# Optimization experiments

Measured on AMD Instinct MI355X. Metric: run time of the kernel, lower is better.

The kernel has to match this reference:

```python
import jax, jax.numpy as jnp
import numpy as np

# Window-batch of 16x16 windows from a U-Net stage
B, C, H, W = 128, 128, 16, 16
HEADS = 8
EQK, EV = 128, 512      # embed_dim_qk, embed_dim_v (embed_dim=512, ratio=4)
L = H * W               # tokens per window (stride=1)


def _conv3x3(x, w, b):
    # NCHW 3x3 conv, padding 1
    out = jax.lax.conv_general_dilated(x, w, (1, 1), ((1, 1), (1, 1)),
                                       dimension_numbers=('NCHW', 'OIHW', 'NCHW'))
    return out + b[None, :, None, None]


def _pos_att(q, wq, bq, wk, bk, wv, bv, wo, bo, gamma):
    # MultiHeadAttention2D_POS, stride=1 -> conv_q/k/v are 1x1 convs
    hd, hdv = EQK // HEADS, EV // HEADS

    def proj(x, w, bias, d):
        y = jnp.einsum('bchw,ec->behw', x, w) + bias[None, :, None, None]
        return y.reshape(B, HEADS, d, L).transpose(0, 1, 3, 2)  # (B,h,L,d)

    pq = proj(q, wq, bq, hd)
    pk = proj(q, wk, bk, hd)
    pv = proj(q, wv, bv, hdv)
    attn = jax.nn.softmax(jnp.einsum('bhqd,bhkd->bhqk', pq, pk) * hd ** -0.5, axis=-1)
    out = jnp.einsum('bhqk,bhkd->bhqd', attn, pv)
    out = out.transpose(0, 1, 3, 2).reshape(B, EV, H, W)
    out = _conv3x3(out, wo, bo)             # proj_out: 3x3 conv EV->C
    return q + out * gamma                  # gamma-scaled residual


def _cha_att(q, wq, bq, wk, bk, wv, bv, wo, bo, gamma):
    # MultiHeadAttention2D_CHA: depthwise 1x1 grouped convs (channel multiplier = HEADS),
    # attention over the CHANNEL axis. Faithfully reproduces torch's reshape of the
    # group-major (c*HEADS+h) channel layout into (B, heads, C, L).
    def dwproj(x, w, bias):
        y = (x[:, :, None] * w.reshape(C, HEADS)[None, :, :, None, None]
             + bias.reshape(C, HEADS)[None, :, :, None, None])
        return y.reshape(B, C * HEADS, H, W).reshape(B, HEADS, C, L)

    pq = dwproj(q, wq, bq)
    pk = dwproj(q, wk, bk)
    pv = dwproj(q, wv, bv)
    attn = jax.nn.softmax(jnp.einsum('bhcl,bhdl->bhcd', pq, pk) * L ** -0.5, axis=-1)
    out = jnp.einsum('bhcd,bhdl->bhcl', attn, pv)      # (B,h,C,L)
    out = out.reshape(B, HEADS * C, H, W)
    # proj_out: grouped 1x1 ConvTranspose (== grouped 1x1 conv): sum each HEADS-sized group
    out = (out.reshape(B, C, HEADS, H, W)
           * wo.reshape(C, HEADS)[None, :, :, None, None]).sum(2) + bo[None, :, None, None]
    return q + out * gamma


def _forward(qkv_pos, qkv_cha,
             pos_wq, pos_bq, pos_wk, pos_bk, pos_wv, pos_bv, pos_wo, pos_bo, gamma_pos,
             cha_wq, cha_bq, cha_wk, cha_bk, cha_wv, cha_bv, cha_wo, cha_bo, gamma_cha,
             fuse_w, fuse_b):
    out_pos = _pos_att(qkv_pos, pos_wq, pos_bq, pos_wk, pos_bk, pos_wv, pos_bv,
                       pos_wo, pos_bo, gamma_pos)
    out_cha = _cha_att(qkv_cha, cha_wq, cha_bq, cha_wk, cha_bk, cha_wv, cha_bv,
                       cha_wo, cha_bo, gamma_cha)
    out = (out_pos + out_cha) * 0.5          # att_fusion='add' (slides=0 -> full slices)
    return _conv3x3(out, fuse_w, fuse_b)     # conv_out (Dropout2d is identity at eval)


def setup_inputs() -> dict:
    key = jax.random.key(0)
    ks = jax.random.split(key, 24)
    n = lambda k, shape, s=0.05: jax.random.normal(k, shape, dtype=jnp.float32) * s
    return {
        'qkv_pos': jax.random.normal(ks[0], (B, C, H, W), jnp.float32),
        'qkv_cha': jax.random.normal(ks[1], (B, C, H, W), jnp.float32),
        'pos_wq': n(ks[2], (EQK, C)), 'pos_bq': n(ks[3], (EQK,)),
        'pos_wk': n(ks[4], (EQK, C)), 'pos_bk': n(ks[5], (EQK,)),
        'pos_wv': n(ks[6], (EV, C)), 'pos_bv': n(ks[7], (EV,)),
        'pos_wo': n(ks[8], (C, EV, 3, 3)), 'pos_bo': n(ks[9], (C,)),
        'gamma_pos': jnp.array(0.1, jnp.float32),
        'cha_wq': n(ks[10], (C * HEADS,)), 'cha_bq': n(ks[11], (C * HEADS,)),
        'cha_wk': n(ks[12], (C * HEADS,)), 'cha_bk': n(ks[13], (C * HEADS,)),
        'cha_wv': n(ks[14], (C * HEADS,)), 'cha_bv': n(ks[15], (C * HEADS,)),
        'cha_wo': n(ks[16], (C * HEADS,)), 'cha_bo': n(ks[17], (C,)),
        'gamma_cha': jnp.array(0.1, jnp.float32),
        'fuse_w': n(ks[18], (C, C, 3, 3)), 'fuse_b': n(ks[19], (C,)),
    }


def reference(qkv_pos, qkv_cha,
              pos_wq, pos_bq, pos_wk, pos_bk, pos_wv, pos_bv, pos_wo, pos_bo, gamma_pos,
              cha_wq, cha_bq, cha_wk, cha_bk, cha_wv, cha_bv, cha_wo, cha_bo, gamma_cha,
              fuse_w, fuse_b):
    return _forward(qkv_pos, qkv_cha,
                    pos_wq, pos_bq, pos_wk, pos_bk, pos_wv, pos_bv, pos_wo, pos_bo, gamma_pos,
                    cha_wq, cha_bq, cha_wk, cha_bk, cha_wv, cha_bv, cha_wo, cha_bo, gamma_cha,
                    fuse_w, fuse_b)
```

## Files before the change

### kernel.cpp

```cpp
#include <hip/hip_runtime.h>
#include <cstdint>
#include <cstddef>

typedef unsigned short ushort_t;
typedef unsigned int uint_t;
typedef __attribute__((ext_vector_type(8))) short bf16x8;
typedef __attribute__((ext_vector_type(4))) float f32x4;

#define NB 128
#define NC 128
#define NL 256
#define NH 8
#define HD 16
#define HDV 64
#define NEV 512
#define PHALF 4194304

__device__ __forceinline__ ushort_t f2bf(float f) {
    uint_t u = __float_as_uint(f);
    u += 0x7fffu + ((u >> 16) & 1u);
    return (ushort_t)(u >> 16);
}
__device__ __forceinline__ float bf2f(ushort_t s) {
    return __uint_as_float(((uint_t)s) << 16);
}
__device__ __forceinline__ uint_t pack2(float lo, float hi) {
    uint_t r;
    asm("v_cvt_pk_bf16_f32 %0, %1, %2" : "=v"(r) : "v"(lo), "v"(hi));
    return r;
}

template<int CIN>
__global__ __launch_bounds__(256) void k_wpack(const float* __restrict__ w,
                                               short* __restrict__ wp) {
    int idx = blockIdx.x * 256 + threadIdx.x;
    if (idx >= CIN * 1152) return;
    int j    = idx & 7;
    int lane = (idx >> 3) & 63;
    int frag = idx >> 9;
    int rt   = frag & 7;
    int tap  = (frag >> 3) % 9;
    int ch   = frag / 72;
    int co   = rt * 16 + (lane & 15);
    int g    = lane >> 4;
    int ci   = ch * 32 + g * 8 + j;
    wp[idx] = (short)f2bf(w[((size_t)co * CIN + ci) * 9 + tap]);
}

template<int E>
__global__ __launch_bounds__(256) void k_wpack_qkv(const float* __restrict__ w,
                                                   short* __restrict__ wp) {
    int idx = blockIdx.x * 256 + threadIdx.x;
    if (idx >= E * 128) return;
    int j    = idx & 7;
    int lane = (idx >> 3) & 63;
    int ch   = (idx >> 9) & 3;
    int rt   = idx >> 11;
    int n = lane & 15, g = lane >> 4;
    wp[idx] = (short)f2bf(w[(size_t)(rt*16 + n)*128 + ch*32 + g*8 + j]);
}

__global__ __launch_bounds__(256) void k_xpose(const float* __restrict__ x,
                                               ushort_t* __restrict__ xbf) {
    const int half = blockIdx.x, b = blockIdx.y, t = threadIdx.x;
    const float* src = x + (size_t)b*NC*NL + (size_t)half*64*NL + t;
    uint_t* dst = (uint_t*)(xbf + ((size_t)b*NL + t)*NC + half*64);
    #pragma unroll
    for (int k8 = 0; k8 < 8; ++k8) {
        uint4 u;
        u.x = pack2(src[(k8*8+0)*NL], src[(k8*8+1)*NL]);
        u.y = pack2(src[(k8*8+2)*NL], src[(k8*8+3)*NL]);
        u.z = pack2(src[(k8*8+4)*NL], src[(k8*8+5)*NL]);
        u.w = pack2(src[(k8*8+6)*NL], src[(k8*8+7)*NL]);
        *(uint4*)(dst + k8*4) = u;
    }
}

__global__ __launch_bounds__(512, 4) void k_pos_mfma(
    const ushort_t* __restrict__ xbf,
    const short* __restrict__ wpq, const short* __restrict__ wpk,
    const short* __restrict__ wpv,
    const float* __restrict__ bq, const float* __restrict__ bk,
    const float* __restrict__ bv,
    ushort_t* __restrict__ att)
{
    const int h = blockIdx.x, b = blockIdx.y;
    const int t = threadIdx.x;
    const int lane = t & 63, w = t >> 6;
    const int n = lane & 15, g = lane >> 4;

    __shared__ __align__(16) short lds[26112];

    const f32x4 z4 = {0.f, 0.f, 0.f, 0.f};
    f32x4 qacc[2], kacc[2], vacc[4][2];
    #pragma unroll
    for (int ct = 0; ct < 2; ++ct) { qacc[ct] = z4; kacc[ct] = z4; }
    #pragma unroll
    for (int vt = 0; vt < 4; ++vt)
        #pragma unroll
        for (int ct = 0; ct < 2; ++ct) vacc[vt][ct] = z4;

    const ushort_t* xr = xbf + ((size_t)(b*NL + w*32 + n))*NC;

    #pragma unroll 2
    for (int ch = 0; ch < 4; ++ch) {
        bf16x8 xb[2];
        #pragma unroll
        for (int ct = 0; ct < 2; ++ct)
            xb[ct] = *(const bf16x8*)(xr + ct*16*NC + ch*32 + g*8);
        const size_t fo = ((size_t)((h*4 + ch)*64) + lane) * 8;
        {
            bf16x8 aq = *(const bf16x8*)(wpq + fo);
            #pragma unroll
            for (int ct = 0; ct < 2; ++ct)
                qacc[ct] = __builtin_amdgcn_mfma_f32_16x16x32_bf16(aq, xb[ct], qacc[ct], 0, 0, 0);
        }
        {
            bf16x8 ak = *(const bf16x8*)(wpk + fo);
            #pragma unroll
            for (int ct = 0; ct < 2; ++ct)
                kacc[ct] = __builtin_amdgcn_mfma_f32_16x16x32_bf16(ak, xb[ct], kacc[ct], 0, 0, 0);
        }
        #pragma unroll
        for (int vt = 0; vt < 4; ++vt) {
            bf16x8 av = *(const bf16x8*)(wpv + ((size_t)((((h*4 + vt)*4) + ch)*64) + lane) * 8);
            #pragma unroll
            for (int ct = 0; ct < 2; ++ct)
                vacc[vt][ct] = __builtin_amdgcn_mfma_f32_16x16x32_bf16(xb[ct], av, vacc[vt][ct], 0, 0, 0);
        }
    }

    uint_t qu01[2], qu23[2];
    {
        float bqv[4], bkv[4];
        #pragma unroll
        for (int r = 0; r < 4; ++r) {
            bqv[r] = bq[h*16 + g*4 + r];
            bkv[r] = bk[h*16 + g*4 + r];
        }
        #pragma unroll
        for (int ct = 0; ct < 2; ++ct) {
            qu01[ct] = pack2(qacc[ct][0] + bqv[0], qacc[ct][1] + bqv[1]);
            qu23[ct] = pack2(qacc[ct][2] + bqv[2], qacc[ct][3] + bqv[3]);
            uint2 kp;
            kp.x = pack2(kacc[ct][0] + bkv[0], kacc[ct][1] + bkv[1]);
            kp.y = pack2(kacc[ct][2] + bkv[2], kacc[ct][3] + bkv[3]);
            *(uint2*)&lds[(w*32 + ct*16 + n)*16 + g*4] = kp;
        }
        #pragma unroll
        for (int vt = 0; vt < 4; ++vt) {
            const float bvv = bv[h*64 + vt*16 + n];
            #pragma unroll
            for (int ct = 0; ct < 2; ++ct) {
                uint2 vp;
                vp.x = pack2(vacc[vt][ct][0] + bvv, vacc[vt][ct][1] + bvv);
                vp.y = pack2(vacc[vt][ct][2] + bvv, vacc[vt][ct][3] + bvv);
                *(uint2*)&lds[9216 + (vt*16 + n)*264 + w*32 + ct*16 + g*4] = vp;
            }
        }
    }
    __syncthreads();

    const int a0 = (n + 32*(g & 1)) * 4;
    #pragma unroll 1
    for (int qt = 0; qt < 2; ++qt) {
        union { uint_t u[4]; bf16x8 v; } qfu;
        qfu.u[0] = (uint_t)__builtin_amdgcn_ds_bpermute(a0,      (int)qu01[qt]);
        qfu.u[1] = (uint_t)__builtin_amdgcn_ds_bpermute(a0,      (int)qu23[qt]);
        qfu.u[2] = (uint_t)__builtin_amdgcn_ds_bpermute(a0 + 64, (int)qu01[qt]);
        qfu.u[3] = (uint_t)__builtin_amdgcn_ds_bpermute(a0 + 64, (int)qu23[qt]);
        if (g >= 2) { qfu.u[0] = 0; qfu.u[1] = 0; qfu.u[2] = 0; qfu.u[3] = 0; }
        bf16x8 qf = qfu.v;

        f32x4 s[16];
        #pragma unroll
        for (int kt = 0; kt < 16; ++kt) {
            bf16x8 kf = (bf16x8){0,0,0,0,0,0,0,0};
            if (g < 2) kf = *(const bf16x8*)&lds[(kt*16 + n)*16 + g*8];
            s[kt] = __builtin_amdgcn_mfma_f32_16x16x32_bf16(kf, qf, z4, 0, 0, 0);
        }
        float den = 0.f;
        #pragma unroll
        for (int kt = 0; kt < 16; ++kt)
            #pragma unroll
            for (int r = 0; r < 4; ++r) {
                float e = exp2f(s[kt][r] * 0.36067376022224085f);
                s[kt][r] = e;
                den += e;
            }
        den += __shfl_xor(den, 16);
        den += __shfl_xor(den, 32);
        const float inv = 1.f / den;

        f32x4 oacc[4] = {z4, z4, z4, z4};
        #pragma unroll
        for (int c2 = 0; c2 < 8; ++c2) {
            #pragma unroll
            for (int u = 0; u < 2; ++u) {
                const int kt = 2*c2 + u;
                uint2 pp;
                pp.x = pack2(s[kt][0], s[kt][1]);
                pp.y = pack2(s[kt][2], s[kt][3]);
                *(uint2*)&lds[4096 + w*640 + n*40 + u*16 + g*4] = pp;
            }
            bf16x8 pf = *(const bf16x8*)&lds[4096 + w*640 + n*40 + g*8];
            #pragma unroll
            for (int vt = 0; vt < 4; ++vt) {
                bf16x8 av = *(const bf16x8*)&lds[9216 + (vt*16 + n)*264 + c2*32 + g*8];
                oacc[vt] = __builtin_amdgcn_mfma_f32_16x16x32_bf16(av, pf, oacc[vt], 0, 0, 0);
            }
        }
        ushort_t* ap = att + (((size_t)b*NL + (w*32 + qt*16 + n))*NEV + h*HDV + g*4);
        #pragma unroll
        for (int vt = 0; vt < 4; ++vt) {
            uint2 op;
            op.x = pack2(oacc[vt][0]*inv, oacc[vt][1]*inv);
            op.y = pack2(oacc[vt][2]*inv, oacc[vt][3]*inv);
            *(uint2*)(ap + vt*16) = op;
        }
    }
}

__global__ __launch_bounds__(256, 3) void k_conv_ci(
    const ushort_t* __restrict__ att, const short* __restrict__ wp,
    ushort_t* __restrict__ P)
{
    const int kc = blockIdx.x >> 1, lh = blockIdx.x & 1, b = blockIdx.y;
    const int t = threadIdx.x;
    const int lane = t & 63, w = t >> 6;
    const int wr = w >> 1, wc = w & 1;
    const int n = lane & 15, gl = lane >> 4;
    const int y0 = lh * 8;

    __shared__ __align__(16) short ims[2][5760];

    {
        bf16x8 z = {0,0,0,0,0,0,0,0};
        bf16x8* p = (bf16x8*)&ims[0][0];
        for (int i = t; i < 1440; i += 256) p[i] = z;
    }

    f32x4 acc[4][4];
    #pragma unroll
    for (int i = 0; i < 4; ++i)
        #pragma unroll
        for (int j = 0; j < 4; ++j) acc[i][j] = (f32x4){0.f,0.f,0.f,0.f};

    const int gg1 = t & 3,        xx1 = (t >> 2) & 15,        yp1 = t >> 6;
    const int id2 = t + 256;
    const int gg2 = id2 & 3,      xx2 = (id2 >> 2) & 15,      yp2 = id2 >> 6;
    const int id3 = t + 512;
    const int gg3 = id3 & 3,      xx3 = (id3 >> 2) & 15,      yp3 = id3 >> 6;
    const bool has3 = (t < 128);
    const int y1 = y0 - 1 + yp1, y2 = y0 - 1 + yp2, y3 = y0 - 1 + yp3;
    const bool ok1 = (y1 >= 0) && (y1 < 16);
    const bool ok2 = (y2 >= 0) && (y2 < 16);
    const bool ok3 = has3 && (y3 >= 0) && (y3 < 16);
    const ushort_t* src1 = att + ((size_t)(b*NL + y1*16 + xx1))*NEV + kc*256 + gg1*8;
    const ushort_t* src2 = att + ((size_t)(b*NL + y2*16 + xx2))*NEV + kc*256 + gg2*8;
    const ushort_t* src3 = att + ((size_t)(b*NL + y3*16 + xx3))*NEV + kc*256 + gg3*8;
    const int slot1 = ((yp1*4 + gg1)*18 + xx1 + 1) * 8;
    const int slot2 = ((yp2*4 + gg2)*18 + xx2 + 1) * 8;
    const int slot3 = ((yp3*4 + gg3)*18 + xx3 + 1) * 8;

    bf16x8 v1 = {0,0,0,0,0,0,0,0}, v2 = v1, v3 = v1;
    if (ok1) v1 = *(const bf16x8*)src1;
    if (ok2) v2 = *(const bf16x8*)src2;
    if (ok3) v3 = *(const bf16x8*)src3;
    __syncthreads();

    #pragma unroll 1
    for (int ch = 0; ch < 8; ++ch) {
        short* buf = &ims[ch & 1][0];
        *(bf16x8*)&buf[slot1] = v1;
        *(bf16x8*)&buf[slot2] = v2;
        if (has3) *(bf16x8*)&buf[slot3] = v3;
        if (ch < 7) {
            if (ok1) v1 = *(const bf16x8*)(src1 + (ch + 1) * 32);
            if (ok2) v2 = *(const bf16x8*)(src2 + (ch + 1) * 32);
            if (ok3) v3 = *(const bf16x8*)(src3 + (ch + 1) * 32);
        }
        __syncthreads();
        #pragma unroll
        for (int tap = 0; tap < 9; ++tap) {
            const int dy = tap / 3, dx = tap % 3;
            bf16x8 Bf[4];
            #pragma unroll
            for (int ct = 0; ct < 4; ++ct)
                Bf[ct] = *(const bf16x8*)&buf[(((wc*4 + ct + dy)*4 + gl)*18 + n + dx) * 8];
            bf16x8 Af[4];
            #pragma unroll
            for (int rt = 0; rt < 4; ++rt)
                Af[rt] = *(const bf16x8*)(wp +
                    ((size_t)(((kc*8 + ch)*9 + tap)*8 + wr*4 + rt)) * 512 + lane*8);
            #pragma unroll
            for (int rt = 0; rt < 4; ++rt)
                #pragma unroll
                for (int ct = 0; ct < 4; ++ct)
                    acc[rt][ct] = __builtin_amdgcn_mfma_f32_16x16x32_bf16(
                        Af[rt], Bf[ct], acc[rt][ct], 0, 0, 0);
        }
    }

    ushort_t* Pb = P + (size_t)kc * PHALF + (size_t)b * NL * NC;
    #pragma unroll
    for (int rt = 0; rt < 4; ++rt) {
        const int co0 = wr*64 + rt*16 + gl*4;
        #pragma unroll
        for (int ct = 0; ct < 4; ++ct) {
            const int l = lh*128 + wc*64 + ct*16 + n;
            uint2 u;
            u.x = pack2(acc[rt][ct][0], acc[rt][ct][1]);
            u.y = pack2(acc[rt][ct][2], acc[rt][ct][3]);
            *(uint2*)(Pb + (size_t)l*NC + co0) = u;
        }
    }
}

__global__ __launch_bounds__(256, 3) void k_conv_co(
    const float* __restrict__ comb, const short* __restrict__ wp,
    const float* __restrict__ bias, float* __restrict__ out)
{
    const int kc = blockIdx.x >> 1, lh = blockIdx.x & 1, b = blockIdx.y;
    const int t = threadIdx.x;
    const int lane = t & 63, w = t >> 6;
    const int wr = w >> 1, wc = w & 1;
    const int n = lane & 15, gl = lane >> 4;
    const int y0 = lh * 8;

    __shared__ __align__(16) short ims[2][5760];

    {
        bf16x8 z = {0,0,0,0,0,0,0,0};
        bf16x8* p = (bf16x8*)&ims[0][0];
        for (int i = t; i < 1440; i += 256) p[i] = z;
    }

    f32x4 acc[2][4];
    #pragma unroll
    for (int i = 0; i < 2; ++i)
        #pragma unroll
        for (int j = 0; j < 4; ++j) acc[i][j] = (f32x4){0.f,0.f,0.f,0.f};

    const int gg1 = t & 3,        xx1 = (t >> 2) & 15,        yp1 = t >> 6;
    const int id2 = t + 256;
    const int gg2 = id2 & 3,      xx2 = (id2 >> 2) & 15,      yp2 = id2 >> 6;
    const int id3 = t + 512;
    const int gg3 = id3 & 3,      xx3 = (id3 >> 2) & 15,      yp3 = id3 >> 6;
    const bool has3 = (t < 128);
    const int y1 = y0 - 1 + yp1, y2 = y0 - 1 + yp2, y3 = y0 - 1 + yp3;
    const bool ok1 = (y1 >= 0) && (y1 < 16);
    const bool ok2 = (y2 >= 0) && (y2 < 16);
    const bool ok3 = has3 && (y3 >= 0) && (y3 < 16);
    const float* s1 = comb + ((size_t)(b*NL + y1*16 + xx1))*NC + gg1*8;
    const float* s2 = comb + ((size_t)(b*NL + y2*16 + xx2))*NC + gg2*8;
    const float* s3 = comb + ((size_t)(b*NL + y3*16 + xx3))*NC + gg3*8;
    const int slot1 = ((yp1*4 + gg1)*18 + xx1 + 1) * 8;
    const int slot2 = ((yp2*4 + gg2)*18 + xx2 + 1) * 8;
    const int slot3 = ((yp3*4 + gg3)*18 + xx3 + 1) * 8;

    float4 f1a, f1b, f2a, f2b, f3a, f3b;
    f1a = f1b = f2a = f2b = f3a = f3b = (float4){0.f,0.f,0.f,0.f};
    if (ok1) { f1a = *(const float4*)s1; f1b = *(const float4*)(s1 + 4); }
    if (ok2) { f2a = *(const float4*)s2; f2b = *(const float4*)(s2 + 4); }
    if (ok3) { f3a = *(const float4*)s3; f3b = *(const float4*)(s3 + 4); }
    __syncthreads();

    #pragma unroll 1
    for (int ch = 0; ch < 4; ++ch) {
        short* buf = &ims[ch & 1][0];
        uint4 w1, w2, w3;
        w1.x = pack2(f1a.x, f1a.y);  w1.y = pack2(f1a.z, f1a.w);
        w1.z = pack2(f1b.x, f1b.y);  w1.w = pack2(f1b.z, f1b.w);
        w2.x = pack2(f2a.x, f2a.y);  w2.y = pack2(f2a.z, f2a.w);
        w2.z = pack2(f2b.x, f2b.y);  w2.w = pack2(f2b.z, f2b.w);
        w3.x = pack2(f3a.x, f3a.y);  w3.y = pack2(f3a.z, f3a.w);
        w3.z = pack2(f3b.x, f3b.y);  w3.w = pack2(f3b.z, f3b.w);
        *(uint4*)&buf[slot1] = w1;
        *(uint4*)&buf[slot2] = w2;
        if (has3) *(uint4*)&buf[slot3] = w3;
        if (ch < 3) {
            if (ok1) { f1a = *(const float4*)(s1 + (ch+1)*32); f1b = *(const float4*)(s1 + (ch+1)*32 + 4); }
            if (ok2) { f2a = *(const float4*)(s2 + (ch+1)*32); f2b = *(const float4*)(s2 + (ch+1)*32 + 4); }
            if (ok3) { f3a = *(const float4*)(s3 + (ch+1)*32); f3b = *(const float4*)(s3 + (ch+1)*32 + 4); }
        }
        __syncthreads();
        #pragma unroll
        for (int tap = 0; tap < 9; ++tap) {
            const int dy = tap / 3, dx = tap % 3;
            bf16x8 Bf[4];
            #pragma unroll
            for (int ct = 0; ct < 4; ++ct)
                Bf[ct] = *(const bf16x8*)&buf[(((wc*4 + ct + dy)*4 + gl)*18 + n + dx) * 8];
            bf16x8 Af[2];
            #pragma unroll
            for (int rt = 0; rt < 2; ++rt)
                Af[rt] = *(const bf16x8*)(wp +
                    ((size_t)((ch*9 + tap)*8 + kc*4 + wr*2 + rt)) * 512 + lane*8);
            #pragma unroll
            for (int rt = 0; rt < 2; ++rt)
                #pragma unroll
                for (int ct = 0; ct < 4; ++ct)
                    acc[rt][ct] = __builtin_amdgcn_mfma_f32_16x16x32_bf16(
                        Af[rt], Bf[ct], acc[rt][ct], 0, 0, 0);
        }
    }

    #pragma unroll
    for (int rt = 0; rt < 2; ++rt) {
        const int co0 = kc*64 + wr*32 + rt*16 + gl*4;
        const float c0 = bias[co0+0], c1 = bias[co0+1],
                    c2 = bias[co0+2], c3 = bias[co0+3];
        #pragma unroll
        for (int ct = 0; ct < 4; ++ct) {
            const int l = lh*128 + wc*64 + ct*16 + n;
            f32x4 a = acc[rt][ct];
            out[((size_t)b*NC + co0+0)*NL + l] = c0 + a[0];
            out[((size_t)b*NC + co0+1)*NL + l] = c1 + a[1];
            out[((size_t)b*NC + co0+2)*NL + l] = c2 + a[2];
            out[((size_t)b*NC + co0+3)*NL + l] = c3 + a[3];
        }
    }
}

#define NLP 260
__global__ __launch_bounds__(256) void k_cha(
    const float* __restrict__ xc,
    const float* __restrict__ cwq, const float* __restrict__ cbq,
    const float* __restrict__ cwk, const float* __restrict__ cbk,
    const float* __restrict__ cwv, const float* __restrict__ cbv,
    const float* __restrict__ cwo, const float* __restrict__ cbo,
    const float* __restrict__ gamma,
    const ushort_t* __restrict__ P, const float* __restrict__ qpos,
    const float* __restrict__ pbo, const float* __restrict__ gpos,
    float* __restrict__ comb)
{
    const int h = blockIdx.x, b = blockIdx.y, t = threadIdx.x;
    __shared__ float qh[16][NLP];
    __shared__ float G_s[16][17];
    __shared__ float S_s[16];
    __shared__ float wq_s[128], bq_s[128], wk_s[128], bk_s[128], wv_s[128], bv_s[128];
    __shared__ float A_s[128][17];
    __shared__ float B_s[128];
    __shared__ float M_s[16][17];
    __shared__ float c_s[16];

    #pragma unroll
    for (int j = 0; j < 16; ++j)
        qh[j][t] = xc[((size_t)b*NC + h*16 + j)*NL + t];
    if (t < 128) {
        const int k = h*128 + t;
        wq_s[t] = cwq[k]; bq_s[t] = cbq[k];
        wk_s[t] = cwk[k]; bk_s[t] = cbk[k];
        wv_s[t] = cwv[k]; bv_s[t] = cbv[k];
    }
    __syncthreads();
    {
        const int i = t >> 4, j = t & 15;
        const float4* qi = (const float4*)qh[i];
        const float4* qj = (const float4*)qh[j];
        float gg = 0.f;
        for (int l4 = 0; l4 < NL/4; ++l4) {
            float4 a = qi[l4], c = qj[l4];
            gg = fmaf(a.x,c.x,fmaf(a.y,c.y,fmaf(a.z,c.z,fmaf(a.w,c.w,gg))));
        }
        G_s[i][j] = gg;
    }
    if (t < 16) {
        const float4* qi = (const float4*)qh[t];
        float s = 0.f;
        for (int l4 = 0; l4 < NL/4; ++l4) { float4 a = qi[l4]; s += a.x + a.y + a.z + a.w; }
        S_s[t] = s;
    }
    __syncthreads();
    if (t < 128) {
        const int c2 = t, cg = c2 >> 3;
        const float wqc = wq_s[c2], bqc = bq_s[c2];
        float Pv[16];
        #pragma unroll
        for (int j = 0; j < 16; ++j) Pv[j] = wqc*G_s[cg][j] + bqc*S_s[j];
        const float Qc = wqc*S_s[cg] + bqc*256.0f;
        float mx = -3.0e38f;
        #pragma unroll
        for (int dg = 0; dg < 16; ++dg) {
            #pragma unroll
            for (int dj = 0; dj < 8; ++dj) {
                const int d = dg*8 + dj;
                float s = wk_s[d]*Pv[dg] + bk_s[d]*Qc;
                mx = fmaxf(mx, s);
            }
        }
        float A[16];
        #pragma unroll
        for (int j = 0; j < 16; ++j) A[j] = 0.f;
        float Bv = 0.f, den = 0.f;
        #pragma unroll
        for (int dg = 0; dg < 16; ++dg) {
            #pragma unroll
            for (int dj = 0; dj < 8; ++dj) {
                const int d = dg*8 + dj;
                float s = wk_s[d]*Pv[dg] + bk_s[d]*Qc;
                float e = __expf((s - mx) * 0.0625f);
                den += e;
                A[dg] = fmaf(e, wv_s[d], A[dg]);
                Bv = fmaf(e, bv_s[d], Bv);
            }
        }
        const float inv = 1.f / den;
        #pragma unroll
        for (int j = 0; j < 16; ++j) A_s[c2][j] = A[j]*inv;
        B_s[c2] = Bv*inv;
    }
    __syncthreads();
    {
        const int cl = t >> 4, j = t & 15;
        const int cp = h*16 + cl;
        float m = 0.f;
        #pragma unroll
        for (int hp = 0; hp < 8; ++hp)
            m = fmaf(cwo[cp*8+hp], A_s[cl*8+hp][j], m);
        M_s[cl][j] = m;
        if (j == 0) {
            float cc = cbo[cp];
            #pragma unroll
            for (int hp = 0; hp < 8; ++hp)
                cc = fmaf(cwo[cp*8+hp], B_s[cl*8+hp], cc);
            c_s[cl] = cc;
        }
    }
    __syncthreads();
    {
        const float g  = gamma[0];
        const float gp = gpos[0];
        const int l = t;
        float av[16];
        #pragma unroll
        for (int cl = 0; cl < 16; ++cl) {
            float a = c_s[cl];
            #pragma unroll
            for (int j = 0; j < 16; ++j)
                a = fmaf(M_s[cl][j], qh[j][l], a);
            av[cl] = a;
        }
        const ushort_t* p0 = P + ((size_t)b*NL + l)*NC + h*16;
        const ushort_t* p1 = p0 + PHALF;
        const float* qp = qpos + ((size_t)b*NC + h*16)*NL + l;
        float4* cp4 = (float4*)(comb + ((size_t)b*NL + l)*NC + h*16);
        #pragma unroll
        for (int q = 0; q < 4; ++q) {
            uint2 u0 = *(const uint2*)(p0 + 4*q);
            uint2 u1 = *(const uint2*)(p1 + 4*q);
            float s0 = bf2f((ushort_t)(u0.x & 0xffffu)) + bf2f((ushort_t)(u1.x & 0xffffu));
            float s1 = bf2f((ushort_t)(u0.x >> 16))     + bf2f((ushort_t)(u1.x >> 16));
            float s2 = bf2f((ushort_t)(u0.y & 0xffffu)) + bf2f((ushort_t)(u1.y & 0xffffu));
            float s3 = bf2f((ushort_t)(u0.y >> 16))     + bf2f((ushort_t)(u1.y >> 16));
            float4 c;
            c.x = 0.5f*(qp[(4*q+0)*NL] + gp*(pbo[h*16+4*q+0] + s0) + qh[4*q+0][l] + g*av[4*q+0]);
            c.y = 0.5f*(qp[(4*q+1)*NL] + gp*(pbo[h*16+4*q+1] + s1) + qh[4*q+1][l] + g*av[4*q+1]);
            c.z = 0.5f*(qp[(4*q+2)*NL] + gp*(pbo[h*16+4*q+2] + s2) + qh[4*q+2][l] + g*av[4*q+2]);
            c.w = 0.5f*(qp[(4*q+3)*NL] + gp*(pbo[h*16+4*q+3] + s3) + qh[4*q+3][l] + g*av[4*q+3]);
            cp4[q] = c;
        }
    }
}

extern "C" void kernel_launch(void* const* d_in, const int* in_sizes, int n_in,
                              void* d_out, int out_size, void* d_ws, size_t ws_size,
                              hipStream_t stream)
{
    const float* qpos = (const float*)d_in[0];
    const float* qcha = (const float*)d_in[1];
    const float* pwq  = (const float*)d_in[2];
    const float* pbq  = (const float*)d_in[3];
    const float* pwk  = (const float*)d_in[4];
    const float* pbk  = (const float*)d_in[5];
    const float* pwv  = (const float*)d_in[6];
    const float* pbv  = (const float*)d_in[7];
    const float* pwo  = (const float*)d_in[8];
    const float* pbo  = (const float*)d_in[9];
    const float* gpos = (const float*)d_in[10];
    const float* cwq  = (const float*)d_in[11];
    const float* cbq  = (const float*)d_in[12];
    const float* cwk  = (const float*)d_in[13];
    const float* cbk  = (const float*)d_in[14];
    const float* cwv  = (const float*)d_in[15];
    const float* cbv  = (const float*)d_in[16];
    const float* cwo  = (const float*)d_in[17];
    const float* cbo  = (const float*)d_in[18];
    const float* gcha = (const float*)d_in[19];
    const float* fw   = (const float*)d_in[20];
    const float* fb   = (const float*)d_in[21];
    float* outp = (float*)d_out;

    char* ws = (char*)d_ws;
    ushort_t* att  = (ushort_t*)ws;
    float*    comb = (float*)ws;
    ushort_t* P    = (ushort_t*)(ws + 33554432);
    ushort_t* xbf  = (ushort_t*)(ws + 33554432);
    short*    wp1  = (short*)(ws + 50331648);
    short*    wp2  = (short*)(ws + 51511296);
    short*    wpq  = (short*)(ws + 51806208);
    short*    wpk  = (short*)(ws + 51838976);
    short*    wpv  = (short*)(ws + 51871744);

    k_wpack<NEV><<<dim3((NEV*1152 + 255)/256), 256, 0, stream>>>(pwo, wp1);
    k_wpack<NC ><<<dim3((NC *1152 + 255)/256), 256, 0, stream>>>(fw,  wp2);
    k_wpack_qkv<128><<<dim3(64),  256, 0, stream>>>(pwq, wpq);
    k_wpack_qkv<128><<<dim3(64),  256, 0, stream>>>(pwk, wpk);
    k_wpack_qkv<512><<<dim3(256), 256, 0, stream>>>(pwv, wpv);

    k_xpose<<<dim3(2, NB), 256, 0, stream>>>(qpos, xbf);
    k_pos_mfma<<<dim3(NH, NB), 512, 0, stream>>>(xbf, wpq, wpk, wpv,
                                                 pbq, pbk, pbv, att);
    k_conv_ci<<<dim3(4, NB), 256, 0, stream>>>(att, wp1, P);
    k_cha<<<dim3(NH, NB), 256, 0, stream>>>(qcha, cwq, cbq, cwk, cbk, cwv, cbv,
                                            cwo, cbo, gcha,
                                            P, qpos, pbo, gpos, comb);
    k_conv_co<<<dim3(4, NB), 256, 0, stream>>>(comb, wp2, fb, outp);
}
```

Measured before the change: 175.2 us.

## Process full 16x16 window per conv block and reuse B rows across dy taps

Both 3x3 conv kernels now have each block cover the whole 16x16 window instead of half of it, which halves the grid and removes the halo rows that were loaded twice. Each wave loads 10 input rows once per dx and reuses them across the three dy taps, doubling the per-wave output tile to 8 column tiles. The softmax exponent sum in the attention kernel is also split into four independent accumulators to shorten the dependency chain. In exchange, accumulator register use roughly doubles and the launch bound drops to one block per SM, lowering occupancy with fewer blocks in flight.

```diff
diff --git a/kernel.cpp b/kernel.cpp
--- a/kernel.cpp
+++ b/kernel.cpp
@@ -179,15 +179,17 @@
             if (g < 2) kf = *(const bf16x8*)&lds[(kt*16 + n)*16 + g*8];
             s[kt] = __builtin_amdgcn_mfma_f32_16x16x32_bf16(kf, qf, z4, 0, 0, 0);
         }
-        float den = 0.f;
-        #pragma unroll
-        for (int kt = 0; kt < 16; ++kt)
-            #pragma unroll
-            for (int r = 0; r < 4; ++r) {
-                float e = exp2f(s[kt][r] * 0.36067376022224085f);
-                s[kt][r] = e;
-                den += e;
-            }
+        float d0 = 0.f, d1 = 0.f, d2 = 0.f, d3 = 0.f;
+        #pragma unroll
+        for (int kt = 0; kt < 16; ++kt) {
+            float e0 = exp2f(s[kt][0] * 0.36067376022224085f);
+            float e1 = exp2f(s[kt][1] * 0.36067376022224085f);
+            float e2 = exp2f(s[kt][2] * 0.36067376022224085f);
+            float e3 = exp2f(s[kt][3] * 0.36067376022224085f);
+            s[kt][0] = e0; s[kt][1] = e1; s[kt][2] = e2; s[kt][3] = e3;
+            d0 += e0; d1 += e1; d2 += e2; d3 += e3;
+        }
+        float den = (d0 + d1) + (d2 + d3);
         den += __shfl_xor(den, 16);
         den += __shfl_xor(den, 32);
         const float inv = 1.f / den;
@@ -221,84 +223,77 @@
     }
 }
 
-__global__ __launch_bounds__(256, 3) void k_conv_ci(
+__global__ __launch_bounds__(256, 1) void k_conv_ci(
     const ushort_t* __restrict__ att, const short* __restrict__ wp,
     ushort_t* __restrict__ P)
 {
-    const int kc = blockIdx.x >> 1, lh = blockIdx.x & 1, b = blockIdx.y;
+    const int kc = blockIdx.x, b = blockIdx.y;
     const int t = threadIdx.x;
     const int lane = t & 63, w = t >> 6;
     const int wr = w >> 1, wc = w & 1;
     const int n = lane & 15, gl = lane >> 4;
-    const int y0 = lh * 8;
-
-    __shared__ __align__(16) short ims[2][5760];
+
+    __shared__ __align__(16) short ims[2][10368];
 
     {
         bf16x8 z = {0,0,0,0,0,0,0,0};
         bf16x8* p = (bf16x8*)&ims[0][0];
-        for (int i = t; i < 1440; i += 256) p[i] = z;
-    }
-
-    f32x4 acc[4][4];
+        for (int i = t; i < 2592; i += 256) p[i] = z;
+    }
+
+    f32x4 acc[4][8];
     #pragma unroll
     for (int i = 0; i < 4; ++i)
         #pragma unroll
-        for (int j = 0; j < 4; ++j) acc[i][j] = (f32x4){0.f,0.f,0.f,0.f};
-
-    const int gg1 = t & 3,        xx1 = (t >> 2) & 15,        yp1 = t >> 6;
-    const int id2 = t + 256;
-    const int gg2 = id2 & 3,      xx2 = (id2 >> 2) & 15,      yp2 = id2 >> 6;
-    const int id3 = t + 512;
-    const int gg3 = id3 & 3,      xx3 = (id3 >> 2) & 15,      yp3 = id3 >> 6;
-    const bool has3 = (t < 128);
-    const int y1 = y0 - 1 + yp1, y2 = y0 - 1 + yp2, y3 = y0 - 1 + yp3;
-    const bool ok1 = (y1 >= 0) && (y1 < 16);
-    const bool ok2 = (y2 >= 0) && (y2 < 16);
-    const bool ok3 = has3 && (y3 >= 0) && (y3 < 16);
-    const ushort_t* src1 = att + ((size_t)(b*NL + y1*16 + xx1))*NEV + kc*256 + gg1*8;
-    const ushort_t* src2 = att + ((size_t)(b*NL + y2*16 + xx2))*NEV + kc*256 + gg2*8;
-    const ushort_t* src3 = att + ((size_t)(b*NL + y3*16 + xx3))*NEV + kc*256 + gg3*8;
-    const int slot1 = ((yp1*4 + gg1)*18 + xx1 + 1) * 8;
-    const int slot2 = ((yp2*4 + gg2)*18 + xx2 + 1) * 8;
-    const int slot3 = ((yp3*4 + gg3)*18 + xx3 + 1) * 8;
-
-    bf16x8 v1 = {0,0,0,0,0,0,0,0}, v2 = v1, v3 = v1;
-    if (ok1) v1 = *(const bf16x8*)src1;
-    if (ok2) v2 = *(const bf16x8*)src2;
-    if (ok3) v3 = *(const bf16x8*)src3;
+        for (int j = 0; j < 8; ++j) acc[i][j] = (f32x4){0.f,0.f,0.f,0.f};
+
+    const ushort_t* abase = att + (size_t)b*NL*NEV + kc*256;
+    int soff[4], slots[4];
+    #pragma unroll
+    for (int i = 0; i < 4; ++i) {
+        int id = t + 256*i;
+        int gg = id & 3, xx = (id >> 2) & 15, yy = id >> 6;
+        soff[i]  = (yy*16 + xx)*NEV + gg*8;
+        slots[i] = (((yy+1)*4 + gg)*18 + xx + 1) * 8;
+    }
+
+    bf16x8 pre[4];
+    #pragma unroll
+    for (int i = 0; i < 4; ++i) pre[i] = *(const bf16x8*)(abase + soff[i]);
     __syncthreads();
 
+    const int ybase = wc * 8;
     #pragma unroll 1
     for (int ch = 0; ch < 8; ++ch) {
         short* buf = &ims[ch & 1][0];
-        *(bf16x8*)&buf[slot1] = v1;
-        *(bf16x8*)&buf[slot2] = v2;
-        if (has3) *(bf16x8*)&buf[slot3] = v3;
+        #pragma unroll
+        for (int i = 0; i < 4; ++i) *(bf16x8*)&buf[slots[i]] = pre[i];
         if (ch < 7) {
-            if (ok1) v1 = *(const bf16x8*)(src1 + (ch + 1) * 32);
-            if (ok2) v2 = *(const bf16x8*)(src2 + (ch + 1) * 32);
-            if (ok3) v3 = *(const bf16x8*)(src3 + (ch + 1) * 32);
+            #pragma unroll
+            for (int i = 0; i < 4; ++i)
+                pre[i] = *(const bf16x8*)(abase + soff[i] + (ch + 1)*32);
         }
         __syncthreads();
         #pragma unroll
-        for (int tap = 0; tap < 9; ++tap) {
-            const int dy = tap / 3, dx = tap % 3;
-            bf16x8 Bf[4];
-            #pragma unroll
-            for (int ct = 0; ct < 4; ++ct)
-                Bf[ct] = *(const bf16x8*)&buf[(((wc*4 + ct + dy)*4 + gl)*18 + n + dx) * 8];
-            bf16x8 Af[4];
-            #pragma unroll
-            for (int rt = 0; rt < 4; ++rt)
-                Af[rt] = *(const bf16x8*)(wp +
-                    ((size_t)(((kc*8 + ch)*9 + tap)*8 + wr*4 + rt)) * 512 + lane*8);
-            #pragma unroll
-            for (int rt = 0; rt < 4; ++rt)
+        for (int dx = 0; dx < 3; ++dx) {
+            bf16x8 Brow[10];
+            #pragma unroll
+            for (int r = 0; r < 10; ++r)
+                Brow[r] = *(const bf16x8*)&buf[(((ybase + r)*4 + gl)*18 + n + dx) * 8];
+            #pragma unroll
+            for (int dy = 0; dy < 3; ++dy) {
+                bf16x8 Af[4];
                 #pragma unroll
-                for (int ct = 0; ct < 4; ++ct)
-                    acc[rt][ct] = __builtin_amdgcn_mfma_f32_16x16x32_bf16(
-                        Af[rt], Bf[ct], acc[rt][ct], 0, 0, 0);
+                for (int rt = 0; rt < 4; ++rt)
+                    Af[rt] = *(const bf16x8*)(wp +
+                        ((size_t)(((kc*8 + ch)*9 + dy*3 + dx)*8 + wr*4 + rt)) * 512 + lane*8);
+                #pragma unroll
+                for (int ct = 0; ct < 8; ++ct)
+                    #pragma unroll
+                    for (int rt = 0; rt < 4; ++rt)
+                        acc[rt][ct] = __builtin_amdgcn_mfma_f32_16x16x32_bf16(
+                            Af[rt], Brow[ct + dy], acc[rt][ct], 0, 0, 0);
+            }
         }
     }
 
@@ -307,8 +302,8 @@
     for (int rt = 0; rt < 4; ++rt) {
         const int co0 = wr*64 + rt*16 + gl*4;
         #pragma unroll
-        for (int ct = 0; ct < 4; ++ct) {
-            const int l = lh*128 + wc*64 + ct*16 + n;
+        for (int ct = 0; ct < 8; ++ct) {
+            const int l = wc*128 + ct*16 + n;
             uint2 u;
             u.x = pack2(acc[rt][ct][0], acc[rt][ct][1]);
             u.y = pack2(acc[rt][ct][2], acc[rt][ct][3]);
@@ -317,103 +312,98 @@
     }
 }
 
-__global__ __launch_bounds__(256, 3) void k_conv_co(
+__global__ __launch_bounds__(256, 1) void k_conv_co(
     const float* __restrict__ comb, const short* __restrict__ wp,
     const float* __restrict__ bias, float* __restrict__ out)
 {
-    const int kc = blockIdx.x >> 1, lh = blockIdx.x & 1, b = blockIdx.y;
+    const int coh = blockIdx.x, b = blockIdx.y;
     const int t = threadIdx.x;
     const int lane = t & 63, w = t >> 6;
     const int wr = w >> 1, wc = w & 1;
     const int n = lane & 15, gl = lane >> 4;
-    const int y0 = lh * 8;
-
-    __shared__ __align__(16) short ims[2][5760];
+
+    __shared__ __align__(16) short ims[2][10368];
 
     {
         bf16x8 z = {0,0,0,0,0,0,0,0};
         bf16x8* p = (bf16x8*)&ims[0][0];
-        for (int i = t; i < 1440; i += 256) p[i] = z;
-    }
-
-    f32x4 acc[2][4];
+        for (int i = t; i < 2592; i += 256) p[i] = z;
+    }
+
+    f32x4 acc[2][8];
     #pragma unroll
     for (int i = 0; i < 2; ++i)
         #pragma unroll
-        for (int j = 0; j < 4; ++j) acc[i][j] = (f32x4){0.f,0.f,0.f,0.f};
-
-    const int gg1 = t & 3,        xx1 = (t >> 2) & 15,        yp1 = t >> 6;
-    const int id2 = t + 256;
-    const int gg2 = id2 & 3,      xx2 = (id2 >> 2) & 15,      yp2 = id2 >> 6;
-    const int id3 = t + 512;
-    const int gg3 = id3 & 3,      xx3 = (id3 >> 2) & 15,      yp3 = id3 >> 6;
-    const bool has3 = (t < 128);
-    const int y1 = y0 - 1 + yp1, y2 = y0 - 1 + yp2, y3 = y0 - 1 + yp3;
-    const bool ok1 = (y1 >= 0) && (y1 < 16);
-    const bool ok2 = (y2 >= 0) && (y2 < 16);
-    const bool ok3 = has3 && (y3 >= 0) && (y3 < 16);
-    const float* s1 = comb + ((size_t)(b*NL + y1*16 + xx1))*NC + gg1*8;
-    const float* s2 = comb + ((size_t)(b*NL + y2*16 + xx2))*NC + gg2*8;
-    const float* s3 = comb + ((size_t)(b*NL + y3*16 + xx3))*NC + gg3*8;
-    const int slot1 = ((yp1*4 + gg1)*18 + xx1 + 1) * 8;
-    const int slot2 = ((yp2*4 + gg2)*18 + xx2 + 1) * 8;
-    const int slot3 = ((yp3*4 + gg3)*18 + xx3 + 1) * 8;
-
-    float4 f1a, f1b, f2a, f2b, f3a, f3b;
-    f1a = f1b = f2a = f2b = f3a = f3b = (float4){0.f,0.f,0.f,0.f};
-    if (ok1) { f1a = *(const float4*)s1; f1b = *(const float4*)(s1 + 4); }
-    if (ok2) { f2a = *(const float4*)s2; f2b = *(const float4*)(s2 + 4); }
-    if (ok3) { f3a = *(const float4*)s3; f3b = *(const float4*)(s3 + 4); }
+        for (int j = 0; j < 8; ++j) acc[i][j] = (f32x4){0.f,0.f,0.f,0.f};
+
+    const float* cbase = comb + (size_t)b*NL*NC;
+    int soff[4], slots[4];
+    #pragma unroll
+    for (int i = 0; i < 4; ++i) {
+        int id = t + 256*i;
+        int gg = id & 3, xx = (id >> 2) & 15, yy = id >> 6;
+        soff[i]  = (yy*16 + xx)*NC + gg*8;
+        slots[i] = (((yy+1)*4 + gg)*18 + xx + 1) * 8;
+    }
+
+    float4 pa[4], pb[4];
+    #pragma unroll
+    for (int i = 0; i < 4; ++i) {
+        pa[i] = *(const float4*)(cbase + soff[i]);
+        pb[i] = *(const float4*)(cbase + soff[i] + 4);
+    }
     __syncthreads();
 
+    const int ybase = wc * 8;
     #pragma unroll 1
     for (int ch = 0; ch < 4; ++ch) {
         short* buf = &ims[ch & 1][0];
-        uint4 w1, w2, w3;
-        w1.x = pack2(f1a.x, f1a.y);  w1.y = pack2(f1a.z, f1a.w);
-        w1.z = pack2(f1b.x, f1b.y);  w1.w = pack2(f1b.z, f1b.w);
-        w2.x = pack2(f2a.x, f2a.y);  w2.y = pack2(f2a.z, f2a.w);
-        w2.z = pack2(f2b.x, f2b.y);  w2.w = pack2(f2b.z, f2b.w);
-        w3.x = pack2(f3a.x, f3a.y);  w3.y = pack2(f3a.z, f3a.w);
-        w3.z = pack2(f3b.x, f3b.y);  w3.w = pack2(f3b.z, f3b.w);
-        *(uint4*)&buf[slot1] = w1;
-        *(uint4*)&buf[slot2] = w2;
-        if (has3) *(uint4*)&buf[slot3] = w3;
+        #pragma unroll
+        for (int i = 0; i < 4; ++i) {
+            uint4 u;
+            u.x = pack2(pa[i].x, pa[i].y);  u.y = pack2(pa[i].z, pa[i].w);
+            u.z = pack2(pb[i].x, pb[i].y);  u.w = pack2(pb[i].z, pb[i].w);
+            *(uint4*)&buf[slots[i]] = u;
+        }
         if (ch < 3) {
-            if (ok1) { f1a = *(const float4*)(s1 + (ch+1)*32); f1b = *(const float4*)(s1 + (ch+1)*32 + 4); }
-            if (ok2) { f2a = *(const float4*)(s2 + (ch+1)*32); f2b = *(const float4*)(s2 + (ch+1)*32 + 4); }
-            if (ok3) { f3a = *(const float4*)(s3 + (ch+1)*32); f3b = *(const float4*)(s3 + (ch+1)*32 + 4); }
+            #pragma unroll
+            for (int i = 0; i < 4; ++i) {
+                pa[i] = *(const float4*)(cbase + soff[i] + (ch + 1)*32);
+                pb[i] = *(const float4*)(cbase + soff[i] + (ch + 1)*32 + 4);
+            }
         }
         __syncthreads();
         #pragma unroll
-        for (int tap = 0; tap < 9; ++tap) {
-            const int dy = tap / 3, dx = tap % 3;
-            bf16x8 Bf[4];
-            #pragma unroll
-            for (int ct = 0; ct < 4; ++ct)
-                Bf[ct] = *(const bf16x8*)&buf[(((wc*4 + ct + dy)*4 + gl)*18 + n + dx) * 8];
-            bf16x8 Af[2];
-            #pragma unroll
-            for (int rt = 0; rt < 2; ++rt)
-                Af[rt] = *(const bf16x8*)(wp +
-                    ((size_t)((ch*9 + tap)*8 + kc*4 + wr*2 + rt)) * 512 + lane*8);
-            #pragma unroll
-            for (int rt = 0; rt < 2; ++rt)
+        for (int dx = 0; dx < 3; ++dx) {
+            bf16x8 Brow[10];
+            #pragma unroll
+            for (int r = 0; r < 10; ++r)
+                Brow[r] = *(const bf16x8*)&buf[(((ybase + r)*4 + gl)*18 + n + dx) * 8];
+            #pragma unroll
+            for (int dy = 0; dy < 3; ++dy) {
+                bf16x8 Af[2];
                 #pragma unroll
-                for (int ct = 0; ct < 4; ++ct)
-                    acc[rt][ct] = __builtin_amdgcn_mfma_f32_16x16x32_bf16(
-                        Af[rt], Bf[ct], acc[rt][ct], 0, 0, 0);
+                for (int rt = 0; rt < 2; ++rt)
+                    Af[rt] = *(const bf16x8*)(wp +
+                        ((size_t)((ch*9 + dy*3 + dx)*8 + coh*4 + wr*2 + rt)) * 512 + lane*8);
+                #pragma unroll
+                for (int ct = 0; ct < 8; ++ct)
+                    #pragma unroll
+                    for (int rt = 0; rt < 2; ++rt)
+                        acc[rt][ct] = __builtin_amdgcn_mfma_f32_16x16x32_bf16(
+                            Af[rt], Brow[ct + dy], acc[rt][ct], 0, 0, 0);
+            }
         }
     }
 
     #pragma unroll
     for (int rt = 0; rt < 2; ++rt) {
-        const int co0 = kc*64 + wr*32 + rt*16 + gl*4;
+        const int co0 = coh*64 + wr*32 + rt*16 + gl*4;
         const float c0 = bias[co0+0], c1 = bias[co0+1],
                     c2 = bias[co0+2], c3 = bias[co0+3];
         #pragma unroll
-        for (int ct = 0; ct < 4; ++ct) {
-            const int l = lh*128 + wc*64 + ct*16 + n;
+        for (int ct = 0; ct < 8; ++ct) {
+            const int l = wc*128 + ct*16 + n;
             f32x4 a = acc[rt][ct];
             out[((size_t)b*NC + co0+0)*NL + l] = c0 + a[0];
             out[((size_t)b*NC + co0+1)*NL + l] = c1 + a[1];
@@ -612,9 +602,9 @@
     k_xpose<<<dim3(2, NB), 256, 0, stream>>>(qpos, xbf);
     k_pos_mfma<<<dim3(NH, NB), 512, 0, stream>>>(xbf, wpq, wpk, wpv,
                                                  pbq, pbk, pbv, att);
-    k_conv_ci<<<dim3(4, NB), 256, 0, stream>>>(att, wp1, P);
+    k_conv_ci<<<dim3(2, NB), 256, 0, stream>>>(att, wp1, P);
     k_cha<<<dim3(NH, NB), 256, 0, stream>>>(qcha, cwq, cbq, cwk, cbk, cwv, cbv,
                                             cwo, cbo, gcha,
                                             P, qpos, pbo, gpos, comb);
-    k_conv_co<<<dim3(4, NB), 256, 0, stream>>>(comb, wp2, fb, outp);
-}
+    k_conv_co<<<dim3(2, NB), 256, 0, stream>>>(comb, wp2, fb, outp);
+}
```

New measurement: 178.4 us. No clear change (+1.8%).

## Double-buffer conv weight and im2col fragments across taps; split softmax sum accumulators

Applied to the files above, without the earlier changes.

Both 3x3 conv kernels now register double-buffer their operands. They prefetch the next tap's weight fragments from global memory and its LDS B-fragments while the current tap's MFMAs run, and they carry the first weight fragment across channel chunks. The launch-bounds occupancy hint drops from 3 to 2 to make room for the extra registers. The attention softmax splits its denominator into four independent accumulators to shorten the dependency chain. The trade-off is fewer resident waves per CU in exchange for hiding global and LDS latency behind the matrix work.

```diff
diff --git a/kernel.cpp b/kernel.cpp
--- a/kernel.cpp
+++ b/kernel.cpp
@@ -179,15 +179,17 @@
             if (g < 2) kf = *(const bf16x8*)&lds[(kt*16 + n)*16 + g*8];
             s[kt] = __builtin_amdgcn_mfma_f32_16x16x32_bf16(kf, qf, z4, 0, 0, 0);
         }
-        float den = 0.f;
-        #pragma unroll
-        for (int kt = 0; kt < 16; ++kt)
-            #pragma unroll
-            for (int r = 0; r < 4; ++r) {
-                float e = exp2f(s[kt][r] * 0.36067376022224085f);
-                s[kt][r] = e;
-                den += e;
-            }
+        float d0 = 0.f, d1 = 0.f, d2 = 0.f, d3 = 0.f;
+        #pragma unroll
+        for (int kt = 0; kt < 16; ++kt) {
+            float e0 = exp2f(s[kt][0] * 0.36067376022224085f);
+            float e1 = exp2f(s[kt][1] * 0.36067376022224085f);
+            float e2 = exp2f(s[kt][2] * 0.36067376022224085f);
+            float e3 = exp2f(s[kt][3] * 0.36067376022224085f);
+            s[kt][0] = e0; s[kt][1] = e1; s[kt][2] = e2; s[kt][3] = e3;
+            d0 += e0; d1 += e1; d2 += e2; d3 += e3;
+        }
+        float den = (d0 + d1) + (d2 + d3);
         den += __shfl_xor(den, 16);
         den += __shfl_xor(den, 32);
         const float inv = 1.f / den;
@@ -221,7 +223,7 @@
     }
 }
 
-__global__ __launch_bounds__(256, 3) void k_conv_ci(
+__global__ __launch_bounds__(256, 2) void k_conv_ci(
     const ushort_t* __restrict__ att, const short* __restrict__ wp,
     ushort_t* __restrict__ P)
 {
@@ -267,6 +269,15 @@
     if (ok1) v1 = *(const bf16x8*)src1;
     if (ok2) v2 = *(const bf16x8*)src2;
     if (ok3) v3 = *(const bf16x8*)src3;
+
+    const short* wpl = wp + (size_t)lane * 8;
+    bf16x8 Ac[4], An[4], Bc[4], Bn[4];
+    #pragma unroll
+    for (int i = 0; i < 4; ++i) { An[i] = (bf16x8){0,0,0,0,0,0,0,0}; Bn[i] = An[i]; Bc[i] = An[i]; }
+    #pragma unroll
+    for (int rt = 0; rt < 4; ++rt)
+        Ac[rt] = *(const bf16x8*)(wpl + ((size_t)((kc*8*9)*8 + wr*4 + rt)) * 512);
+
     __syncthreads();
 
     #pragma unroll 1
@@ -282,23 +293,36 @@
         }
         __syncthreads();
         #pragma unroll
+        for (int ct = 0; ct < 4; ++ct)
+            Bc[ct] = *(const bf16x8*)&buf[(((wc*4 + ct)*4 + gl)*18 + n) * 8];
+        #pragma unroll
         for (int tap = 0; tap < 9; ++tap) {
-            const int dy = tap / 3, dx = tap % 3;
-            bf16x8 Bf[4];
-            #pragma unroll
-            for (int ct = 0; ct < 4; ++ct)
-                Bf[ct] = *(const bf16x8*)&buf[(((wc*4 + ct + dy)*4 + gl)*18 + n + dx) * 8];
-            bf16x8 Af[4];
-            #pragma unroll
-            for (int rt = 0; rt < 4; ++rt)
-                Af[rt] = *(const bf16x8*)(wp +
-                    ((size_t)(((kc*8 + ch)*9 + tap)*8 + wr*4 + rt)) * 512 + lane*8);
+            if (tap < 8) {
+                const int dy = (tap + 1) / 3, dx = (tap + 1) % 3;
+                #pragma unroll
+                for (int rt = 0; rt < 4; ++rt)
+                    An[rt] = *(const bf16x8*)(wpl +
+                        ((size_t)(((kc*8 + ch)*9 + tap + 1)*8 + wr*4 + rt)) * 512);
+                #pragma unroll
+                for (int ct = 0; ct < 4; ++ct)
+                    Bn[ct] = *(const bf16x8*)&buf[(((wc*4 + ct + dy)*4 + gl)*18 + n + dx) * 8];
+            } else if (ch < 7) {
+                #pragma unroll
+                for (int rt = 0; rt < 4; ++rt)
+                    An[rt] = *(const bf16x8*)(wpl +
+                        ((size_t)(((kc*8 + ch + 1)*9)*8 + wr*4 + rt)) * 512);
+            }
             #pragma unroll
             for (int rt = 0; rt < 4; ++rt)
                 #pragma unroll
                 for (int ct = 0; ct < 4; ++ct)
                     acc[rt][ct] = __builtin_amdgcn_mfma_f32_16x16x32_bf16(
-                        Af[rt], Bf[ct], acc[rt][ct], 0, 0, 0);
+                        Ac[rt], Bc[ct], acc[rt][ct], 0, 0, 0);
+            #pragma unroll
+            for (int i = 0; i < 4; ++i) {
+                if (tap < 8 || ch < 7) Ac[i] = An[i];
+                if (tap < 8)           Bc[i] = Bn[i];
+            }
         }
     }
 
@@ -317,7 +341,7 @@
     }
 }
 
-__global__ __launch_bounds__(256, 3) void k_conv_co(
+__global__ __launch_bounds__(256, 2) void k_conv_co(
     const float* __restrict__ comb, const short* __restrict__ wp,
     const float* __restrict__ bias, float* __restrict__ out)
 {
@@ -364,6 +388,17 @@
     if (ok1) { f1a = *(const float4*)s1; f1b = *(const float4*)(s1 + 4); }
     if (ok2) { f2a = *(const float4*)s2; f2b = *(const float4*)(s2 + 4); }
     if (ok3) { f3a = *(const float4*)s3; f3b = *(const float4*)(s3 + 4); }
+
+    const short* wpl = wp + (size_t)lane * 8;
+    bf16x8 Ac[2], An[2], Bc[4], Bn[4];
+    #pragma unroll
+    for (int i = 0; i < 2; ++i) An[i] = (bf16x8){0,0,0,0,0,0,0,0};
+    #pragma unroll
+    for (int i = 0; i < 4; ++i) { Bn[i] = (bf16x8){0,0,0,0,0,0,0,0}; Bc[i] = Bn[i]; }
+    #pragma unroll
+    for (int rt = 0; rt < 2; ++rt)
+        Ac[rt] = *(const bf16x8*)(wpl + ((size_t)(kc*4 + wr*2 + rt)) * 512);
+
     __syncthreads();
 
     #pragma unroll 1
@@ -386,23 +421,37 @@
         }
         __syncthreads();
         #pragma unroll
+        for (int ct = 0; ct < 4; ++ct)
+            Bc[ct] = *(const bf16x8*)&buf[(((wc*4 + ct)*4 + gl)*18 + n) * 8];
+        #pragma unroll
         for (int tap = 0; tap < 9; ++tap) {
-            const int dy = tap / 3, dx = tap % 3;
-            bf16x8 Bf[4];
-            #pragma unroll
-            for (int ct = 0; ct < 4; ++ct)
-                Bf[ct] = *(const bf16x8*)&buf[(((wc*4 + ct + dy)*4 + gl)*18 + n + dx) * 8];
-            bf16x8 Af[2];
-            #pragma unroll
-            for (int rt = 0; rt < 2; ++rt)
-                Af[rt] = *(const bf16x8*)(wp +
-                    ((size_t)((ch*9 + tap)*8 + kc*4 + wr*2 + rt)) * 512 + lane*8);
+            if (tap < 8) {
+                const int dy = (tap + 1) / 3, dx = (tap + 1) % 3;
+                #pragma unroll
+                for (int rt = 0; rt < 2; ++rt)
+                    An[rt] = *(const bf16x8*)(wpl +
+                        ((size_t)((ch*9 + tap + 1)*8 + kc*4 + wr*2 + rt)) * 512);
+                #pragma unroll
+                for (int ct = 0; ct < 4; ++ct)
+                    Bn[ct] = *(const bf16x8*)&buf[(((wc*4 + ct + dy)*4 + gl)*18 + n + dx) * 8];
+            } else if (ch < 3) {
+                #pragma unroll
+                for (int rt = 0; rt < 2; ++rt)
+                    An[rt] = *(const bf16x8*)(wpl +
+                        ((size_t)((ch + 1)*9*8 + kc*4 + wr*2 + rt)) * 512);
+            }
             #pragma unroll
             for (int rt = 0; rt < 2; ++rt)
                 #pragma unroll
                 for (int ct = 0; ct < 4; ++ct)
                     acc[rt][ct] = __builtin_amdgcn_mfma_f32_16x16x32_bf16(
-                        Af[rt], Bf[ct], acc[rt][ct], 0, 0, 0);
+                        Ac[rt], Bc[ct], acc[rt][ct], 0, 0, 0);
+            #pragma unroll
+            for (int i = 0; i < 2; ++i)
+                if (tap < 8 || ch < 3) Ac[i] = An[i];
+            #pragma unroll
+            for (int i = 0; i < 4; ++i)
+                if (tap < 8) Bc[i] = Bn[i];
         }
     }
 
```

Measured after the change: 172.1 us. Within noise of the previous version (-1.8%).
